# Performance work log

Measured on AMD Instinct MI355X. Metric: run time of the kernel, lower is better.

Reference implementation:

```python
import jax, jax.numpy as jnp
import numpy as np

B, N, DIN, D, L, H = 8, 1024, 768, 384, 6, 12
HD = D // H
STD = 0.02
EPS = 1e-5


def setup_inputs() -> dict:
    key = jax.random.key(0)
    ks = jax.random.split(key, 24)
    inp = {}
    inp["x"] = jax.random.normal(ks[0], (B, N, DIN), jnp.float32)
    inp["height_ids"] = jax.random.randint(ks[1], (B, N), 0, 48)
    inp["width_ids"] = jax.random.randint(ks[2], (B, N), 0, 48)
    inp["target_mask"] = jax.random.randint(ks[3], (B, N), 0, 2).astype(bool)
    inp["sequence_ids"] = jnp.sort(jax.random.randint(ks[4], (B, N), 0, 8), axis=-1)
    inp["sequence_mask"] = (jax.random.randint(ks[5], (B, N), 0, 10) > 8)
    inp["r"] = 0
    # parameters (weights stored [in, out]; y = x @ W + b)
    inp["embed_w"] = jax.random.normal(ks[6], (DIN, D), jnp.float32) * STD
    inp["embed_b"] = jnp.zeros((D,), jnp.float32)
    inp["h_embed"] = jax.random.normal(ks[7], (48, D), jnp.float32) * STD
    inp["w_embed"] = jax.random.normal(ks[8], (48, D), jnp.float32) * STD
    inp["mask_token"] = jax.random.normal(ks[9], (D,), jnp.float32) * STD
    rescale = (1.0 / jnp.sqrt(2.0 * (jnp.arange(L) + 1.0))).astype(jnp.float32)
    inp["norm1_w"] = jnp.ones((L, D), jnp.float32)
    inp["norm1_b"] = jnp.zeros((L, D), jnp.float32)
    inp["ls1"] = 1e-5 * jnp.ones((L, D), jnp.float32)
    inp["qkv_w"] = jax.random.normal(ks[10], (L, D, 3 * D), jnp.float32) * STD
    inp["qkv_b"] = jnp.zeros((L, 3 * D), jnp.float32)
    inp["proj_w"] = jax.random.normal(ks[11], (L, D, D), jnp.float32) * STD * rescale[:, None, None]
    inp["proj_b"] = jnp.zeros((L, D), jnp.float32)
    inp["norm2_w"] = jnp.ones((L, D), jnp.float32)
    inp["norm2_b"] = jnp.zeros((L, D), jnp.float32)
    inp["fc1_w"] = jax.random.normal(ks[12], (L, D, 4 * D), jnp.float32) * STD
    inp["fc1_b"] = jnp.zeros((L, 4 * D), jnp.float32)
    inp["fc2_w"] = jax.random.normal(ks[13], (L, 4 * D, D), jnp.float32) * STD * rescale[:, None, None]
    inp["fc2_b"] = jnp.zeros((L, D), jnp.float32)
    inp["ls2"] = 1e-5 * jnp.ones((L, D), jnp.float32)
    inp["pnorm_w"] = jnp.ones((D,), jnp.float32)
    inp["pnorm_b"] = jnp.zeros((D,), jnp.float32)
    inp["pproj_w"] = jax.random.normal(ks[14], (D, DIN), jnp.float32) * STD
    inp["pproj_b"] = jnp.zeros((DIN,), jnp.float32)
    return inp


def _layernorm(x, w, b):
    mu = jnp.mean(x, axis=-1, keepdims=True)
    var = jnp.mean(jnp.square(x - mu), axis=-1, keepdims=True)
    return (x - mu) * jax.lax.rsqrt(var + EPS) * w + b


def _attention(x, attn_mask, qkv_w, qkv_b, proj_w, proj_b):
    # x: [B,N,D]; attn_mask: [B,1,N,N] True where attention is disallowed
    qkv = (x @ qkv_w + qkv_b).reshape(B, N, 3, H, HD).transpose(2, 0, 3, 1, 4)
    q, k, v = qkv[0], qkv[1], qkv[2]  # [B,H,N,HD]
    attn = jnp.einsum("bhnd,bhmd->bhnm", q, k) * (HD ** -0.5)
    neg_inf = jnp.finfo(attn.dtype).min
    attn = jnp.where(attn_mask, neg_inf, attn)
    attn = jax.nn.softmax(attn, axis=-1)
    out = jnp.einsum("bhnm,bhmd->bhnd", attn, v).transpose(0, 2, 1, 3).reshape(B, N, D)
    return out @ proj_w + proj_b


def reference(x, height_ids, width_ids, target_mask, sequence_ids, sequence_mask, r,
              embed_w, embed_b, h_embed, w_embed, mask_token,
              norm1_w, norm1_b, ls1, qkv_w, qkv_b, proj_w, proj_b,
              norm2_w, norm2_b, fc1_w, fc1_b, fc2_w, fc2_b, ls2,
              pnorm_w, pnorm_b, pproj_w, pproj_b):
    h = x @ embed_w + embed_b
    tm = target_mask[..., None]
    h = jnp.where(tm, mask_token, h)
    h = h + h_embed[height_ids] + w_embed[width_ids]
    # packed-sequence block-diagonal mask; True = NOT allowed
    mask = sequence_ids[:, :, None] != sequence_ids[:, None, :]
    mask = mask | sequence_mask[:, :, None] | sequence_mask[:, None, :]
    mask = mask[:, None]  # broadcast over heads: [B,1,N,N]
    for i in range(L):  # r == 0 path: plain blocks, tome is None
        h = h + ls1[i] * _attention(_layernorm(h, norm1_w[i], norm1_b[i]), mask,
                                    qkv_w[i], qkv_b[i], proj_w[i], proj_b[i])
        z = _layernorm(h, norm2_w[i], norm2_b[i])
        z = jax.nn.gelu(z @ fc1_w[i] + fc1_b[i], approximate=False) @ fc2_w[i] + fc2_b[i]
        h = h + ls2[i] * z
    h = _layernorm(h, pnorm_w, pnorm_b)
    return h @ pproj_w + pproj_b
```

## Files before the change

### kernel.cpp

```cpp
#include <hip/hip_runtime.h>
#include <math.h>

#define BB   8
#define NN   1024
#define DIN  768
#define DD   384
#define LL   6
#define HH   12
#define HDD  32
#define MM   (BB*NN)
#define EPSF 1e-5f

typedef __attribute__((ext_vector_type(8))) short short8;
typedef __attribute__((ext_vector_type(4))) float f32x4;

__device__ __forceinline__ unsigned short f2b(float f) {
    unsigned int u = __builtin_bit_cast(unsigned int, f);
    u = (u + 0x7fffu + ((u >> 16) & 1u)) >> 16;
    return (unsigned short)u;
}
__device__ __forceinline__ float b2f(unsigned short h) {
    return __builtin_bit_cast(float, ((unsigned int)h) << 16);
}

__global__ __launch_bounds__(1024) void cvt_mask_k(const void* __restrict__ src,
                                                   int n, int* __restrict__ dst)
{
    __shared__ int flag;
    if (threadIdx.x == 0) flag = 0;
    __syncthreads();
    const int* si = (const int*)src;
    int nq = n >> 2;
    int any = 0;
    for (int i = threadIdx.x; i < nq; i += blockDim.x) any |= si[i] & ~1;
    if (any) atomicOr(&flag, 1);
    __syncthreads();
    if (flag) {
        const unsigned char* sb = (const unsigned char*)src;
        for (int i = threadIdx.x; i < n; i += blockDim.x) dst[i] = sb[i];
    } else {
        for (int i = threadIdx.x; i < n; i += blockDim.x) dst[i] = si[i];
    }
}

__global__ __launch_bounds__(64) void kminmax_k(const int* __restrict__ sids,
                                                const int* __restrict__ smask,
                                                int2* __restrict__ kmm)
{
    int e = blockIdx.x;
    int b = e >> 4, kt = e & 15;
    int lane = threadIdx.x;
    int kk = b * NN + kt * 64 + lane;
    int s = sids[kk];
    int msk = smask[kk];
    int mn = msk ? 0x7fffffff : s;
    int mx = msk ? (int)0x80000000 : s;
    #pragma unroll
    for (int off = 32; off; off >>= 1) {
        mn = min(mn, __shfl_xor(mn, off));
        mx = max(mx, __shfl_xor(mx, off));
    }
    if (lane == 0) kmm[e] = make_int2(mn, mx);
}

__global__ __launch_bounds__(256) void vmean_k(const unsigned short* __restrict__ qkv,
                                               unsigned short* __restrict__ vmean)
{
    __shared__ float part[8][32];
    int bh = blockIdx.x;
    int b = bh / HH, h = bh % HH;
    int d = threadIdx.x & 31, grp = threadIdx.x >> 5;
    const unsigned short* vp = qkv + (size_t)(b * NN + grp * 128) * (3 * DD)
                                   + 2 * DD + h * HDD + d;
    float s = 0.f;
    for (int n = 0; n < 128; ++n)
        s += b2f(vp[(size_t)n * 3 * DD]);
    part[grp][d] = s;
    __syncthreads();
    if (grp == 0) {
        float t = 0.f;
        #pragma unroll
        for (int g2 = 0; g2 < 8; ++g2) t += part[g2][d];
        vmean[bh * HDD + d] = f2b(t * (1.0f / NN));
    }
}

__global__ __launch_bounds__(256) void tcast_k(const float* __restrict__ W,
                                               unsigned short* __restrict__ Wt,
                                               int K, int N)
{
    __shared__ float tile[32][33];
    const size_t lstr = (size_t)K * N;
    const float* Wl = W + blockIdx.z * lstr;
    unsigned short* Wtl = Wt + blockIdx.z * lstr;
    int k0 = blockIdx.x * 32, n0 = blockIdx.y * 32;
    int tx = threadIdx.x & 31, ty = threadIdx.x >> 5;
    #pragma unroll
    for (int r = 0; r < 32; r += 8)
        tile[ty + r][tx] = Wl[(size_t)(k0 + ty + r) * N + n0 + tx];
    __syncthreads();
    #pragma unroll
    for (int r = 0; r < 32; r += 8)
        Wtl[(size_t)(n0 + ty + r) * K + k0 + tx] = f2b(tile[tx][ty + r]);
}

template <int EPI>
__global__ __launch_bounds__(256) void bgemm_k(
    const unsigned short* __restrict__ A, const unsigned short* __restrict__ Wt,
    const float* __restrict__ bias, void* __restrict__ out,
    int K, int NO, const float* __restrict__ ls)
{
    __shared__ unsigned short As[128][40];
    __shared__ unsigned short Bs[128][40];

    const int tid  = threadIdx.x;
    const int lane = tid & 63;
    const int wave = tid >> 6;
    const int wr = wave >> 1, wc = wave & 1;
    const int rowBase = blockIdx.x * 128;
    const int colBase = blockIdx.y * 128;
    const int rr = lane & 15;
    const int kr = (lane >> 4) * 8;

    f32x4 acc[4][4] = {};

    for (int k0 = 0; k0 < K; k0 += 32) {
        #pragma unroll
        for (int i = 0; i < 2; ++i) {
            int s   = tid + i * 256;
            int row = s >> 2;
            int seg = (s & 3) * 8;
            *(short8*)&As[row][seg] =
                *(const short8*)&A[(size_t)(rowBase + row) * K + k0 + seg];
            *(short8*)&Bs[row][seg] =
                *(const short8*)&Wt[(size_t)(colBase + row) * K + k0 + seg];
        }
        __syncthreads();

        short8 af[4], bfr[4];
        #pragma unroll
        for (int i = 0; i < 4; ++i)
            af[i] = *(const short8*)&As[wr * 64 + i * 16 + rr][kr];
        #pragma unroll
        for (int j = 0; j < 4; ++j)
            bfr[j] = *(const short8*)&Bs[wc * 64 + j * 16 + rr][kr];
        #pragma unroll
        for (int i = 0; i < 4; ++i)
            #pragma unroll
            for (int j = 0; j < 4; ++j)
                acc[i][j] = __builtin_amdgcn_mfma_f32_16x16x32_bf16(
                    af[i], bfr[j], acc[i][j], 0, 0, 0);
        __syncthreads();
    }

    const int colq = colBase + wc * 64 + rr;
    const int rq0  = rowBase + wr * 64 + (lane >> 4) * 4;
    #pragma unroll
    for (int j = 0; j < 4; ++j) {
        const int col = colq + j * 16;
        const float bi = bias[col];
        float lsv = 0.f;
        if constexpr (EPI == 2) lsv = ls[col];
        #pragma unroll
        for (int i = 0; i < 4; ++i) {
            #pragma unroll
            for (int r = 0; r < 4; ++r) {
                const int row = rq0 + i * 16 + r;
                float v = acc[i][j][r] + bi;
                if constexpr (EPI == 0) {
                    ((unsigned short*)out)[(size_t)row * NO + col] = f2b(v);
                } else if constexpr (EPI == 2) {
                    float* hp = (float*)out + (size_t)row * NO + col;
                    *hp += lsv * v;
                } else {
                    float g = 0.5f * v * (1.0f + erff(v * 0.70710678118654752f));
                    ((unsigned short*)out)[(size_t)row * NO + col] = f2b(g);
                }
            }
        }
    }
}

template <int EPI>
__global__ __launch_bounds__(256) void gemm_k(
    const float* __restrict__ A, const float* __restrict__ Wt,
    const float* __restrict__ bias, float* __restrict__ C,
    int K, int NO,
    const int* __restrict__ tmask, const int* __restrict__ hids,
    const int* __restrict__ wids, const float* __restrict__ mtok,
    const float* __restrict__ hemb, const float* __restrict__ wemb)
{
    __shared__ float As[16][132];
    __shared__ float Bs[16][64];

    const int tid = threadIdx.x;
    const int tx = tid & 15;
    const int ty = tid >> 4;
    const int rowBase = blockIdx.x * 128;
    const int colBase = blockIdx.y * 64;

    float acc[8][4] = {};

    for (int k0 = 0; k0 < K; k0 += 16) {
        #pragma unroll
        for (int i = 0; i < 2; ++i) {
            int s   = tid + i * 256;
            int row = s >> 2;
            int kq  = (s & 3) * 4;
            float4 av = *(const float4*)(&A[(size_t)(rowBase + row) * K + k0 + kq]);
            As[kq + 0][row] = av.x;
            As[kq + 1][row] = av.y;
            As[kq + 2][row] = av.z;
            As[kq + 3][row] = av.w;
        }
        {
            int r = tid >> 4;
            int c = (tid & 15) * 4;
            *(float4*)(&Bs[r][c]) =
                *(const float4*)(&Wt[(size_t)(k0 + r) * NO + colBase + c]);
        }
        __syncthreads();

        #pragma unroll
        for (int k = 0; k < 16; ++k) {
            float4 b4 = *(const float4*)(&Bs[k][tx * 4]);
            float4 a0 = *(const float4*)(&As[k][ty * 8]);
            float4 a1 = *(const float4*)(&As[k][ty * 8 + 4]);
            float a[8] = {a0.x, a0.y, a0.z, a0.w, a1.x, a1.y, a1.z, a1.w};
            float b[4] = {b4.x, b4.y, b4.z, b4.w};
            #pragma unroll
            for (int i = 0; i < 8; ++i)
                #pragma unroll
                for (int j = 0; j < 4; ++j)
                    acc[i][j] = fmaf(a[i], b[j], acc[i][j]);
        }
        __syncthreads();
    }

    const int cb = colBase + tx * 4;
    float4 bi = *(const float4*)(&bias[cb]);
    #pragma unroll
    for (int i = 0; i < 8; ++i) {
        int r = rowBase + ty * 8 + i;
        float v[4];
        #pragma unroll
        for (int j = 0; j < 4; ++j) v[j] = acc[i][j] + ((const float*)&bi)[j];

        float* cp = &C[(size_t)r * NO + cb];
        if constexpr (EPI == 1) {
            int tm = tmask[r];
            const float* he = &hemb[(size_t)hids[r] * DD + cb];
            const float* we = &wemb[(size_t)wids[r] * DD + cb];
            float4 o;
            #pragma unroll
            for (int j = 0; j < 4; ++j) {
                float x = tm ? mtok[cb + j] : v[j];
                ((float*)&o)[j] = x + he[j] + we[j];
            }
            *(float4*)cp = o;
        } else {
            float4 o = {v[0], v[1], v[2], v[3]};
            *(float4*)cp = o;
        }
    }
}

template <int OUT>
__global__ __launch_bounds__(256) void ln_k(
    const float* __restrict__ X, const float* __restrict__ w,
    const float* __restrict__ b, void* __restrict__ Y)
{
    int row  = blockIdx.x * 4 + (threadIdx.x >> 6);
    int lane = threadIdx.x & 63;
    const float* xr = X + (size_t)row * DD;

    float x[6];
    #pragma unroll
    for (int j = 0; j < 6; ++j) x[j] = xr[lane + 64 * j];

    float s = 0.f;
    #pragma unroll
    for (int j = 0; j < 6; ++j) s += x[j];
    #pragma unroll
    for (int off = 32; off > 0; off >>= 1) s += __shfl_xor(s, off);
    float mu = s * (1.0f / 384.0f);

    float v = 0.f;
    #pragma unroll
    for (int j = 0; j < 6; ++j) { float d = x[j] - mu; v += d * d; }
    #pragma unroll
    for (int off = 32; off > 0; off >>= 1) v += __shfl_xor(v, off);
    float rstd = rsqrtf(v * (1.0f / 384.0f) + EPSF);

    #pragma unroll
    for (int j = 0; j < 6; ++j) {
        int c = lane + 64 * j;
        float y = (x[j] - mu) * rstd * w[c] + b[c];
        if constexpr (OUT == 0) ((float*)Y)[(size_t)row * DD + c] = y;
        else ((unsigned short*)Y)[(size_t)row * DD + c] = f2b(y);
    }
}

__global__ __launch_bounds__(256) void attn_mfma_k(
    const unsigned short* __restrict__ qkv, const int* __restrict__ sids,
    const int* __restrict__ smask, const int2* __restrict__ kmm,
    const unsigned short* __restrict__ vmean, unsigned short* __restrict__ out)
{
    __shared__ unsigned short Vt[32][72];
    __shared__ int ck[64];
    __shared__ unsigned short P[4][16][64];
    __shared__ int qmn[4], qmx[4];

    const int tid  = threadIdx.x;
    const int lane = tid & 63;
    const int wave = tid >> 6;
    const int g = lane >> 4;
    const int c = lane & 15;

    const int bh = blockIdx.x >> 4;
    const int qt = blockIdx.x & 15;
    const int b = bh / HH, h = bh % HH;
    const int q0w = qt * 64 + wave * 16;
    const size_t qrow = 3 * DD;

    const short8 qf = *(const short8*)&qkv[(size_t)(b * NN + q0w + c) * qrow + h * HDD + g * 8];

    int cq[4];
    #pragma unroll
    for (int r = 0; r < 4; ++r) {
        int qq = b * NN + q0w + 4 * g + r;
        cq[r] = smask[qq] ? -2 : sids[qq];
    }

    {
        int lmin = 0x7fffffff, lmax = (int)0x80000000;
        #pragma unroll
        for (int r = 0; r < 4; ++r) {
            if (cq[r] != -2) { lmin = min(lmin, cq[r]); lmax = max(lmax, cq[r]); }
        }
        #pragma unroll
        for (int off = 32; off; off >>= 1) {
            lmin = min(lmin, __shfl_xor(lmin, off));
            lmax = max(lmax, __shfl_xor(lmax, off));
        }
        if (lane == 0) { qmn[wave] = lmin; qmx[wave] = lmax; }
    }
    __syncthreads();
    int qminb = min(min(qmn[0], qmn[1]), min(qmn[2], qmn[3]));
    int qmaxb = max(max(qmx[0], qmx[1]), max(qmx[2], qmx[3]));

    float m[4] = {-INFINITY, -INFINITY, -INFINITY, -INFINITY};
    float l[4] = {};
    f32x4 o[2] = {};
    const f32x4 zero = {};
    const float scale = 0.17677669529663687f;
    const float FMIN = -3.402823466e38f;

    for (int kt = 0; kt < NN / 64; ++kt) {
        const int2 kr = kmm[(b << 4) + kt];
        if (kr.x > qmaxb || kr.y < qminb) continue;

        const int kb = kt * 64;
        {
            int key = tid & 63;
            int d8  = (tid >> 6) * 8;
            short8 v = *(const short8*)&qkv[(size_t)(b * NN + kb + key) * qrow + 2 * DD + h * HDD + d8];
            #pragma unroll
            for (int e = 0; e < 8; ++e)
                Vt[d8 + e][key] = (unsigned short)v[e];
            if (tid < 64) {
                int kk = b * NN + kb + tid;
                ck[tid] = smask[kk] ? -1 : sids[kk];
            }
        }
        __syncthreads();

        f32x4 s4[4];
        #pragma unroll
        for (int j = 0; j < 4; ++j) {
            short8 kf = *(const short8*)&qkv[(size_t)(b * NN + kb + 16 * j + c) * qrow + DD + h * HDD + g * 8];
            s4[j] = __builtin_amdgcn_mfma_f32_16x16x32_bf16(qf, kf, zero, 0, 0, 0);
        }

        float pm[4] = {FMIN, FMIN, FMIN, FMIN};
        #pragma unroll
        for (int j = 0; j < 4; ++j) {
            const int ckj = ck[16 * j + c];
            #pragma unroll
            for (int r = 0; r < 4; ++r) {
                float sv = (cq[r] != ckj) ? FMIN : s4[j][r] * scale;
                s4[j][r] = sv;
                pm[r] = fmaxf(pm[r], sv);
            }
        }
        #pragma unroll
        for (int off = 1; off < 16; off <<= 1)
            #pragma unroll
            for (int r = 0; r < 4; ++r)
                pm[r] = fmaxf(pm[r], __shfl_xor(pm[r], off));

        float fac[4], psum[4];
        #pragma unroll
        for (int r = 0; r < 4; ++r) {
            float mn = fmaxf(m[r], pm[r]);
            fac[r] = __expf(m[r] - mn);
            m[r] = mn;
            psum[r] = 0.f;
        }
        #pragma unroll
        for (int j = 0; j < 4; ++j) {
            #pragma unroll
            for (int r = 0; r < 4; ++r) {
                float p = __expf(s4[j][r] - m[r]);
                psum[r] += p;
                int row  = 4 * g + r;
                int colb = (2 * (16 * j + c)) ^ ((row & 7) << 4);
                *(unsigned short*)((char*)&P[wave][row][0] + colb) = f2b(p);
            }
        }
        #pragma unroll
        for (int off = 1; off < 16; off <<= 1)
            #pragma unroll
            for (int r = 0; r < 4; ++r)
                psum[r] += __shfl_xor(psum[r], off);
        #pragma unroll
        for (int r = 0; r < 4; ++r) l[r] = l[r] * fac[r] + psum[r];

        #pragma unroll
        for (int dc = 0; dc < 2; ++dc)
            #pragma unroll
            for (int r = 0; r < 4; ++r)
                o[dc][r] *= fac[r];

        #pragma unroll
        for (int kc = 0; kc < 2; ++kc) {
            int colb = (2 * (kc * 32 + g * 8)) ^ ((c & 7) << 4);
            short8 pf = *(const short8*)((char*)&P[wave][c][0] + colb);
            #pragma unroll
            for (int dc = 0; dc < 2; ++dc) {
                short8 vf = *(const short8*)&Vt[dc * 16 + c][kc * 32 + g * 8];
                o[dc] = __builtin_amdgcn_mfma_f32_16x16x32_bf16(pf, vf, o[dc], 0, 0, 0);
            }
        }
        __syncthreads();
    }

    #pragma unroll
    for (int r = 0; r < 4; ++r) {
        unsigned short* op = &out[(size_t)(b * NN + q0w + 4 * g + r) * DD + h * HDD];
        if (cq[r] == -2) {
            #pragma unroll
            for (int dc = 0; dc < 2; ++dc)
                op[dc * 16 + c] = vmean[bh * HDD + dc * 16 + c];
        } else {
            const float inv = 1.0f / l[r];
            #pragma unroll
            for (int dc = 0; dc < 2; ++dc)
                op[dc * 16 + c] = f2b(o[dc][r] * inv);
        }
    }
}

extern "C" void kernel_launch(void* const* d_in, const int* in_sizes, int n_in,
                              void* d_out, int out_size, void* d_ws, size_t ws_size,
                              hipStream_t stream)
{
    const float* x        = (const float*)d_in[0];
    const int*   hids     = (const int*)d_in[1];
    const int*   wids     = (const int*)d_in[2];
    const void*  tmask_rw = d_in[3];
    const int*   sids     = (const int*)d_in[4];
    const void*  smask_rw = d_in[5];
    const float* embed_w  = (const float*)d_in[7];
    const float* embed_b  = (const float*)d_in[8];
    const float* h_embed  = (const float*)d_in[9];
    const float* w_embed  = (const float*)d_in[10];
    const float* mtok     = (const float*)d_in[11];
    const float* norm1_w  = (const float*)d_in[12];
    const float* norm1_b  = (const float*)d_in[13];
    const float* ls1      = (const float*)d_in[14];
    const float* qkv_w    = (const float*)d_in[15];
    const float* qkv_b    = (const float*)d_in[16];
    const float* proj_w   = (const float*)d_in[17];
    const float* proj_b   = (const float*)d_in[18];
    const float* norm2_w  = (const float*)d_in[19];
    const float* norm2_b  = (const float*)d_in[20];
    const float* fc1_w    = (const float*)d_in[21];
    const float* fc1_b    = (const float*)d_in[22];
    const float* fc2_w    = (const float*)d_in[23];
    const float* fc2_b    = (const float*)d_in[24];
    const float* ls2      = (const float*)d_in[25];
    const float* pnorm_w  = (const float*)d_in[26];
    const float* pnorm_b  = (const float*)d_in[27];
    const float* pproj_w  = (const float*)d_in[28];
    const float* pproj_b  = (const float*)d_in[29];

    const size_t MD = (size_t)MM * DD;
    float*          h    = (float*)d_ws;
    unsigned short* zb   = (unsigned short*)(h + MD);
    unsigned short* hid  = zb + MD;
    unsigned short* qkvb = hid;
    float*          zf   = (float*)hid;
    unsigned short* wT   = hid + 4 * MD;
    const size_t qkvTsz  = (size_t)LL * 3 * DD * DD;
    const size_t projTsz = (size_t)LL * DD * DD;
    const size_t fc1Tsz  = (size_t)LL * DD * 4 * DD;
    unsigned short* qkvT = wT;
    unsigned short* projT = qkvT + qkvTsz;
    unsigned short* fc1T  = projT + projTsz;
    unsigned short* fc2T  = fc1T + fc1Tsz;
    int* tm32 = (int*)(fc2T + fc1Tsz);
    int* sm32 = tm32 + MM;
    unsigned short* vmean = (unsigned short*)(sm32 + MM);
    int2* kmm = (int2*)(vmean + BB * HH * HDD);

    cvt_mask_k<<<1, 1024, 0, stream>>>(tmask_rw, MM, tm32);
    cvt_mask_k<<<1, 1024, 0, stream>>>(smask_rw, MM, sm32);
    kminmax_k<<<BB * 16, 64, 0, stream>>>(sids, sm32, kmm);

    dim3 t256(256);
    tcast_k<<<dim3(DD/32, 3*DD/32, LL), t256, 0, stream>>>(qkv_w, qkvT, DD, 3*DD);
    tcast_k<<<dim3(DD/32, DD/32,   LL), t256, 0, stream>>>(proj_w, projT, DD, DD);
    tcast_k<<<dim3(DD/32, 4*DD/32, LL), t256, 0, stream>>>(fc1_w, fc1T, DD, 4*DD);
    tcast_k<<<dim3(4*DD/32, DD/32, LL), t256, 0, stream>>>(fc2_w, fc2T, 4*DD, DD);

    gemm_k<1><<<dim3(MM/128, DD/64), t256, 0, stream>>>(
        x, embed_w, embed_b, h, DIN, DD, tm32, hids, wids, mtok, h_embed, w_embed);

    for (int i = 0; i < LL; ++i) {
        ln_k<1><<<MM/4, t256, 0, stream>>>(h, norm1_w + i*DD, norm1_b + i*DD, zb);
        bgemm_k<0><<<dim3(MM/128, 3*DD/128), t256, 0, stream>>>(
            zb, qkvT + (size_t)i*3*DD*DD, qkv_b + i*3*DD, qkvb, DD, 3*DD, nullptr);
        vmean_k<<<BB * HH, t256, 0, stream>>>(qkvb, vmean);
        attn_mfma_k<<<dim3(BB*HH*(NN/64)), t256, 0, stream>>>(
            qkvb, sids, sm32, kmm, vmean, zb);
        bgemm_k<2><<<dim3(MM/128, DD/128), t256, 0, stream>>>(
            zb, projT + (size_t)i*DD*DD, proj_b + i*DD, h, DD, DD, ls1 + i*DD);
        ln_k<1><<<MM/4, t256, 0, stream>>>(h, norm2_w + i*DD, norm2_b + i*DD, zb);
        bgemm_k<3><<<dim3(MM/128, 4*DD/128), t256, 0, stream>>>(
            zb, fc1T + (size_t)i*DD*4*DD, fc1_b + i*4*DD, hid, DD, 4*DD, nullptr);
        bgemm_k<2><<<dim3(MM/128, DD/128), t256, 0, stream>>>(
            hid, fc2T + (size_t)i*4*DD*DD, fc2_b + i*DD, h, 4*DD, DD, ls2 + i*DD);
    }

    ln_k<0><<<MM/4, t256, 0, stream>>>(h, pnorm_w, pnorm_b, zf);
    gemm_k<0><<<dim3(MM/128, DIN/64), t256, 0, stream>>>(
        zf, pproj_w, pproj_b, (float*)d_out, DD, DIN,
        nullptr, nullptr, nullptr, nullptr, nullptr, nullptr);
}
```

Before: 1.352 ms.

## Replace FP32 SIMT embed/output GEMMs with split-bf16 three-pass MFMA GEMMs

The embedding and final projection GEMMs move from FP32 FMA loops to MFMA bf16 instructions. Each FP32 operand is split into high and low bf16 parts, and three MFMA products (lo*hi, hi*lo, hi*hi) rebuild near-FP32 accuracy. Weights are pre-split and transposed by a new cast kernel, and activations are split on the fly while staged into LDS. This trades 3x the MFMA work plus the conversion overhead for much higher matrix-core throughput on these two GEMMs.

```diff
diff --git a/kernel.cpp b/kernel.cpp
--- a/kernel.cpp
+++ b/kernel.cpp
@@ -104,6 +104,133 @@
         Wtl[(size_t)(n0 + ty + r) * K + k0 + tx] = f2b(tile[tx][ty + r]);
 }
 
+__global__ __launch_bounds__(256) void tcast2_k(const float* __restrict__ W,
+                                                unsigned short* __restrict__ WTh,
+                                                unsigned short* __restrict__ WTl,
+                                                int K, int N)
+{
+    __shared__ float tile[32][33];
+    int k0 = blockIdx.x * 32, n0 = blockIdx.y * 32;
+    int tx = threadIdx.x & 31, ty = threadIdx.x >> 5;
+    #pragma unroll
+    for (int r = 0; r < 32; r += 8)
+        tile[ty + r][tx] = W[(size_t)(k0 + ty + r) * N + n0 + tx];
+    __syncthreads();
+    #pragma unroll
+    for (int r = 0; r < 32; r += 8) {
+        float v = tile[tx][ty + r];
+        unsigned short hi = f2b(v);
+        unsigned short lo = f2b(v - b2f(hi));
+        size_t idx = (size_t)(n0 + ty + r) * K + k0 + tx;
+        WTh[idx] = hi;
+        WTl[idx] = lo;
+    }
+}
+
+template <int EPI>
+__global__ __launch_bounds__(256) void sgemm_k(
+    const float* __restrict__ A,
+    const unsigned short* __restrict__ WTh, const unsigned short* __restrict__ WTl,
+    const float* __restrict__ bias, float* __restrict__ out,
+    int K, int NO,
+    const int* __restrict__ tmask, const int* __restrict__ hids,
+    const int* __restrict__ wids, const float* __restrict__ mtok,
+    const float* __restrict__ hemb, const float* __restrict__ wemb)
+{
+    __shared__ unsigned short Ah[128][40];
+    __shared__ unsigned short Al[128][40];
+    __shared__ unsigned short Bh[64][40];
+    __shared__ unsigned short Bl[64][40];
+
+    const int tid  = threadIdx.x;
+    const int lane = tid & 63;
+    const int wave = tid >> 6;
+    const int wr = wave >> 1, wc = wave & 1;
+    const int rowBase = blockIdx.x * 128;
+    const int colBase = blockIdx.y * 64;
+    const int rr = lane & 15;
+    const int kr = (lane >> 4) * 8;
+
+    f32x4 acc[4][2] = {};
+
+    for (int k0 = 0; k0 < K; k0 += 32) {
+        #pragma unroll
+        for (int i = 0; i < 4; ++i) {
+            int s   = tid + i * 256;
+            int row = s >> 3;
+            int q   = (s & 7) * 4;
+            float4 av = *(const float4*)&A[(size_t)(rowBase + row) * K + k0 + q];
+            ushort4 h4, l4;
+            #pragma unroll
+            for (int e = 0; e < 4; ++e) {
+                float v = ((const float*)&av)[e];
+                unsigned short hi = f2b(v);
+                ((unsigned short*)&h4)[e] = hi;
+                ((unsigned short*)&l4)[e] = f2b(v - b2f(hi));
+            }
+            *(ushort4*)&Ah[row][q] = h4;
+            *(ushort4*)&Al[row][q] = l4;
+        }
+        {
+            int s   = tid;
+            int row = s >> 2;
+            int seg = (s & 3) * 8;
+            size_t gi = (size_t)(colBase + row) * K + k0 + seg;
+            *(short8*)&Bh[row][seg] = *(const short8*)&WTh[gi];
+            *(short8*)&Bl[row][seg] = *(const short8*)&WTl[gi];
+        }
+        __syncthreads();
+
+        short8 ah[4], al[4], bh2[2], bl2[2];
+        #pragma unroll
+        for (int i = 0; i < 4; ++i) {
+            ah[i] = *(const short8*)&Ah[wr * 64 + i * 16 + rr][kr];
+            al[i] = *(const short8*)&Al[wr * 64 + i * 16 + rr][kr];
+        }
+        #pragma unroll
+        for (int j = 0; j < 2; ++j) {
+            bh2[j] = *(const short8*)&Bh[wc * 32 + j * 16 + rr][kr];
+            bl2[j] = *(const short8*)&Bl[wc * 32 + j * 16 + rr][kr];
+        }
+        #pragma unroll
+        for (int i = 0; i < 4; ++i)
+            #pragma unroll
+            for (int j = 0; j < 2; ++j) {
+                acc[i][j] = __builtin_amdgcn_mfma_f32_16x16x32_bf16(
+                    al[i], bh2[j], acc[i][j], 0, 0, 0);
+                acc[i][j] = __builtin_amdgcn_mfma_f32_16x16x32_bf16(
+                    ah[i], bl2[j], acc[i][j], 0, 0, 0);
+                acc[i][j] = __builtin_amdgcn_mfma_f32_16x16x32_bf16(
+                    ah[i], bh2[j], acc[i][j], 0, 0, 0);
+            }
+        __syncthreads();
+    }
+
+    const int colq = colBase + wc * 32 + rr;
+    const int rq0  = rowBase + wr * 64 + (lane >> 4) * 4;
+    #pragma unroll
+    for (int j = 0; j < 2; ++j) {
+        const int col = colq + j * 16;
+        const float bi = bias[col];
+        #pragma unroll
+        for (int i = 0; i < 4; ++i) {
+            #pragma unroll
+            for (int r = 0; r < 4; ++r) {
+                const int row = rq0 + i * 16 + r;
+                float v = acc[i][j][r] + bi;
+                if constexpr (EPI == 1) {
+                    float xv = tmask[row] ? mtok[col] : v;
+                    out[(size_t)row * NO + col] = xv
+                        + hemb[(size_t)hids[row] * DD + col]
+                        + wemb[(size_t)wids[row] * DD + col];
+                } else {
+                    out[(size_t)row * NO + col] = v;
+                }
+            }
+        }
+    }
+}
+
 template <int EPI>
 __global__ __launch_bounds__(256) void bgemm_k(
     const unsigned short* __restrict__ A, const unsigned short* __restrict__ Wt,
@@ -177,90 +304,6 @@
                     ((unsigned short*)out)[(size_t)row * NO + col] = f2b(g);
                 }
             }
-        }
-    }
-}
-
-template <int EPI>
-__global__ __launch_bounds__(256) void gemm_k(
-    const float* __restrict__ A, const float* __restrict__ Wt,
-    const float* __restrict__ bias, float* __restrict__ C,
-    int K, int NO,
-    const int* __restrict__ tmask, const int* __restrict__ hids,
-    const int* __restrict__ wids, const float* __restrict__ mtok,
-    const float* __restrict__ hemb, const float* __restrict__ wemb)
-{
-    __shared__ float As[16][132];
-    __shared__ float Bs[16][64];
-
-    const int tid = threadIdx.x;
-    const int tx = tid & 15;
-    const int ty = tid >> 4;
-    const int rowBase = blockIdx.x * 128;
-    const int colBase = blockIdx.y * 64;
-
-    float acc[8][4] = {};
-
-    for (int k0 = 0; k0 < K; k0 += 16) {
-        #pragma unroll
-        for (int i = 0; i < 2; ++i) {
-            int s   = tid + i * 256;
-            int row = s >> 2;
-            int kq  = (s & 3) * 4;
-            float4 av = *(const float4*)(&A[(size_t)(rowBase + row) * K + k0 + kq]);
-            As[kq + 0][row] = av.x;
-            As[kq + 1][row] = av.y;
-            As[kq + 2][row] = av.z;
-            As[kq + 3][row] = av.w;
-        }
-        {
-            int r = tid >> 4;
-            int c = (tid & 15) * 4;
-            *(float4*)(&Bs[r][c]) =
-                *(const float4*)(&Wt[(size_t)(k0 + r) * NO + colBase + c]);
-        }
-        __syncthreads();
-
-        #pragma unroll
-        for (int k = 0; k < 16; ++k) {
-            float4 b4 = *(const float4*)(&Bs[k][tx * 4]);
-            float4 a0 = *(const float4*)(&As[k][ty * 8]);
-            float4 a1 = *(const float4*)(&As[k][ty * 8 + 4]);
-            float a[8] = {a0.x, a0.y, a0.z, a0.w, a1.x, a1.y, a1.z, a1.w};
-            float b[4] = {b4.x, b4.y, b4.z, b4.w};
-            #pragma unroll
-            for (int i = 0; i < 8; ++i)
-                #pragma unroll
-                for (int j = 0; j < 4; ++j)
-                    acc[i][j] = fmaf(a[i], b[j], acc[i][j]);
-        }
-        __syncthreads();
-    }
-
-    const int cb = colBase + tx * 4;
-    float4 bi = *(const float4*)(&bias[cb]);
-    #pragma unroll
-    for (int i = 0; i < 8; ++i) {
-        int r = rowBase + ty * 8 + i;
-        float v[4];
-        #pragma unroll
-        for (int j = 0; j < 4; ++j) v[j] = acc[i][j] + ((const float*)&bi)[j];
-
-        float* cp = &C[(size_t)r * NO + cb];
-        if constexpr (EPI == 1) {
-            int tm = tmask[r];
-            const float* he = &hemb[(size_t)hids[r] * DD + cb];
-            const float* we = &wemb[(size_t)wids[r] * DD + cb];
-            float4 o;
-            #pragma unroll
-            for (int j = 0; j < 4; ++j) {
-                float x = tm ? mtok[cb + j] : v[j];
-                ((float*)&o)[j] = x + he[j] + we[j];
-            }
-            *(float4*)cp = o;
-        } else {
-            float4 o = {v[0], v[1], v[2], v[3]};
-            *(float4*)cp = o;
         }
     }
 }
@@ -513,6 +556,11 @@
     int* sm32 = tm32 + MM;
     unsigned short* vmean = (unsigned short*)(sm32 + MM);
     int2* kmm = (int2*)(vmean + BB * HH * HDD);
+    const size_t ewsz = (size_t)DIN * DD;
+    unsigned short* ewT_hi = (unsigned short*)(kmm + BB * 16);
+    unsigned short* ewT_lo = ewT_hi + ewsz;
+    unsigned short* pwT_hi = ewT_lo + ewsz;
+    unsigned short* pwT_lo = pwT_hi + ewsz;
 
     cvt_mask_k<<<1, 1024, 0, stream>>>(tmask_rw, MM, tm32);
     cvt_mask_k<<<1, 1024, 0, stream>>>(smask_rw, MM, sm32);
@@ -523,9 +571,11 @@
     tcast_k<<<dim3(DD/32, DD/32,   LL), t256, 0, stream>>>(proj_w, projT, DD, DD);
     tcast_k<<<dim3(DD/32, 4*DD/32, LL), t256, 0, stream>>>(fc1_w, fc1T, DD, 4*DD);
     tcast_k<<<dim3(4*DD/32, DD/32, LL), t256, 0, stream>>>(fc2_w, fc2T, 4*DD, DD);
-
-    gemm_k<1><<<dim3(MM/128, DD/64), t256, 0, stream>>>(
-        x, embed_w, embed_b, h, DIN, DD, tm32, hids, wids, mtok, h_embed, w_embed);
+    tcast2_k<<<dim3(DIN/32, DD/32), t256, 0, stream>>>(embed_w, ewT_hi, ewT_lo, DIN, DD);
+    tcast2_k<<<dim3(DD/32, DIN/32), t256, 0, stream>>>(pproj_w, pwT_hi, pwT_lo, DD, DIN);
+
+    sgemm_k<1><<<dim3(MM/128, DD/64), t256, 0, stream>>>(
+        x, ewT_hi, ewT_lo, embed_b, h, DIN, DD, tm32, hids, wids, mtok, h_embed, w_embed);
 
     for (int i = 0; i < LL; ++i) {
         ln_k<1><<<MM/4, t256, 0, stream>>>(h, norm1_w + i*DD, norm1_b + i*DD, zb);
@@ -544,7 +594,7 @@
     }
 
     ln_k<0><<<MM/4, t256, 0, stream>>>(h, pnorm_w, pnorm_b, zf);
-    gemm_k<0><<<dim3(MM/128, DIN/64), t256, 0, stream>>>(
-        zf, pproj_w, pproj_b, (float*)d_out, DD, DIN,
+    sgemm_k<0><<<dim3(MM/128, DIN/64), t256, 0, stream>>>(
+        zf, pwT_hi, pwT_lo, pproj_b, (float*)d_out, DD, DIN,
         nullptr, nullptr, nullptr, nullptr, nullptr, nullptr);
 }
```

New measurement: 1.289 ms. 1.05x faster.
